# Optimization experiments

Measured on AMD Instinct MI355X. Metric: run time of the kernel, lower is better.

## Reference

```python
import jax, jax.numpy as jnp
import numpy as np
from jax.scipy.special import logsumexp

B, DK, N, M = 16, 512, 1024, 1024
SINKHORN_ITERS = 5
EPS = 1e-8


def setup_inputs() -> dict:
    key = jax.random.key(0)
    k1, k2, k3, k4, k5 = jax.random.split(key, 5)
    return {
        "src_embedding": jax.random.normal(k1, (B, DK, N), dtype=jnp.float32),
        "tgt_embedding": jax.random.normal(k2, (B, DK, M), dtype=jnp.float32),
        "src": jax.random.normal(k3, (B, 3, N), dtype=jnp.float32),
        "tgt": jax.random.normal(k4, (B, 3, M), dtype=jnp.float32),
        # temperature must be positive; uniform in [0.05, 1.0)
        "temperature": jax.random.uniform(k5, (B,), dtype=jnp.float32, minval=0.05, maxval=1.0),
    }


def sinkhorn(scores, n_iters):
    # ZeroPad2d((0,1,0,1)): pad one slack row and one slack column with zeros
    scores = jnp.pad(scores, ((0, 0), (0, 1), (0, 1)))
    for _ in range(n_iters):
        # row normalization (all rows except slack row)
        top = scores[:, :-1, :] - logsumexp(scores[:, :-1, :], axis=2, keepdims=True)
        scores = jnp.concatenate([top, scores[:, -1:, :]], axis=1)
        # column normalization (all cols except slack col)
        left = scores[:, :, :-1] - logsumexp(scores[:, :, :-1], axis=1, keepdims=True)
        scores = jnp.concatenate([left, scores[:, :, -1:]], axis=2)
    return scores[:, :-1, :-1]


def reference(src_embedding, tgt_embedding, src, tgt, temperature):
    b, d_k, n = src_embedding.shape
    # [B, N, M] similarity scores
    dists = jnp.einsum('bdn,bdm->bnm', src_embedding, tgt_embedding) / jnp.sqrt(jnp.float32(d_k))
    affinity = dists / temperature[:, None, None]
    log_perm = sinkhorn(affinity, SINKHORN_ITERS)
    perm = jnp.exp(log_perm)                                             # [B,N,M]
    perm_norm = perm / (jnp.sum(perm, axis=2, keepdims=True) + EPS)      # [B,N,M]
    # soft correspondence: weighted_tgt[b,:,i] = sum_j perm_norm[b,i,j] * tgt[b,:,j]
    weighted_tgt = jnp.einsum('bdm,bnm->bdn', tgt, perm_norm)            # [B,3,N]
    weights = jnp.sum(perm, axis=-1, keepdims=True)                      # [B,N,1]
    weights_norm = weights / (jnp.sum(weights, axis=1, keepdims=True) + EPS)
    weights_norm = jnp.swapaxes(weights_norm, 1, 2)                      # [B,1,N]
    src_centroid = jnp.sum(src * weights_norm, axis=2, keepdims=True)    # [B,3,1]
    tgt_centroid = jnp.sum(weighted_tgt * weights_norm, axis=2, keepdims=True)
    src_centered = src - src_centroid
    corr_centered = (weighted_tgt - tgt_centroid) * weights_norm
    # weighted cross-covariance, batched 3x3
    H = jnp.einsum('bin,bjn->bij', src_centered, corr_centered)          # [B,3,3]
    # batched Procrustes via SVD (torch.svd: H = u diag(s) v^T; jnp: H = u diag(s) vh)
    u, s, vh = jnp.linalg.svd(H)
    v = jnp.swapaxes(vh, 1, 2)
    ut = jnp.swapaxes(u, 1, 2)
    r = jnp.matmul(v, ut)
    r_det = jnp.linalg.det(r)                                            # [B]
    diag = jnp.stack([jnp.ones_like(r_det), jnp.ones_like(r_det), r_det], axis=-1)  # [B,3]
    R = jnp.matmul(v * diag[:, None, :], ut)                             # [B,3,3]
    t = (jnp.matmul(-R, src_centroid) + tgt_centroid).reshape(b, 3)
    return R, t, perm_norm
```

## Files before the change

### kernel.cpp

```cpp
#include <hip/hip_runtime.h>
#include <math.h>

#define BB 16
#define NN 1024
#define MM 1024
#define DKK 512
#define RBLK 16
#define NRB  (NN/RBLK)

typedef short short8 __attribute__((ext_vector_type(8)));
typedef float f32x4 __attribute__((ext_vector_type(4)));

__device__ float g_u[BB*NN];
__device__ float g_v[BB*MM];
__device__ float g_w[BB*NN];
__device__ float g_wt[BB*3*NN];
__device__ float g_pm[BB*NRB*MM];
__device__ float g_ps[BB*NRB*MM];
__device__ __attribute__((aligned(16))) unsigned short gAh[BB*NN*DKK];
__device__ __attribute__((aligned(16))) unsigned short gAl[BB*NN*DKK];
__device__ __attribute__((aligned(16))) unsigned short gBh[BB*MM*DKK];
__device__ __attribute__((aligned(16))) unsigned short gBl[BB*MM*DKK];

__global__ __launch_bounds__(256) void zero_v_kernel() {
    int i = blockIdx.x*256 + threadIdx.x;
    if (i < BB*MM) g_v[i] = 0.0f;
}

__device__ __forceinline__ unsigned int bf16_rne(float x){
    unsigned int u = __float_as_uint(x);
    return (u + 0x7fffu + ((u>>16)&1u)) >> 16;
}

__device__ __forceinline__ void gl_lds(const void* g, void* l){
    __builtin_amdgcn_global_load_lds(
        (const __attribute__((address_space(1))) unsigned int*)g,
        (__attribute__((address_space(3))) unsigned int*)l, 16, 0, 0);
}

__global__ __launch_bounds__(256) void convert_split(const float* __restrict__ A,
                                                     const float* __restrict__ Bm) {
    int z = blockIdx.z;
    int which = z >> 4;
    int b = z & 15;
    const float* X = which ? Bm : A;
    unsigned short* Hh = which ? gBh : gAh;
    unsigned short* Hl = which ? gBl : gAl;
    int d0 = blockIdx.y * 64;
    int i0 = blockIdx.x * 64;
    __shared__ float T[64*65];
    const float* Xb = X + ((size_t)b*DKK + d0)*NN + i0;
    int t = threadIdx.x;
#pragma unroll
    for (int it=0; it<4; ++it){
        int lin = t + 256*it;
        int d = lin >> 4;
        int i4 = lin & 15;
        float4 v = *(const float4*)(Xb + (size_t)d*NN + i4*4);
        T[(i4*4+0)*65 + d] = v.x;
        T[(i4*4+1)*65 + d] = v.y;
        T[(i4*4+2)*65 + d] = v.z;
        T[(i4*4+3)*65 + d] = v.w;
    }
    __syncthreads();
    size_t obase = ((size_t)b*NN + i0)*DKK + d0;
#pragma unroll
    for (int it=0; it<2; ++it){
        int c = t + 256*it;
        int i = c >> 3;
        int p = c & 7;
        unsigned int hw[4], lw[4];
#pragma unroll
        for (int j=0;j<4;j++){
            float x0 = T[i*65 + p*8 + 2*j];
            float x1 = T[i*65 + p*8 + 2*j+1];
            unsigned int h0 = bf16_rne(x0);
            unsigned int h1 = bf16_rne(x1);
            float hf0 = __uint_as_float(h0<<16);
            float hf1 = __uint_as_float(h1<<16);
            unsigned int l0 = bf16_rne(x0 - hf0);
            unsigned int l1 = bf16_rne(x1 - hf1);
            hw[j] = h0 | (h1<<16);
            lw[j] = l0 | (l1<<16);
        }
        int pw = (p & 4) | ((p + (i>>1)) & 3);
        size_t eo = obase + (size_t)i*DKK + pw*8;
        uint4 hv; hv.x=hw[0]; hv.y=hw[1]; hv.z=hw[2]; hv.w=hw[3];
        uint4 lv; lv.x=lw[0]; lv.y=lw[1]; lv.z=lw[2]; lv.w=lw[3];
        *(uint4*)(Hh + eo) = hv;
        *(uint4*)(Hl + eo) = lv;
    }
}

__global__ __launch_bounds__(256) void gemm_mfma(const float* __restrict__ temp,
                                                 float* __restrict__ C) {
    int id   = blockIdx.x;
    int xcd  = id & 7;
    int slot = id >> 3;
    int b    = xcd*2 + (slot >> 6);
    int sub  = slot & 63;
    int i0   = (sub >> 3) << 7;
    int j0   = (sub & 7) << 7;
    __shared__ __attribute__((aligned(16))) char lds[65536];
    int t = threadIdx.x;
    int lane = t & 63, w = t >> 6;
    int wr = w >> 1, wc = w & 1;
    const size_t ebytes = (size_t)b * NN * DKK * 2;

    const char* src[8];
    int dstoff[8];
    {
        int rql = lane >> 2, cl = lane & 3;
#pragma unroll
        for (int o=0;o<4;o++){
            const char* g = (o==0) ? (const char*)gAh : (o==1) ? (const char*)gAl
                           : (o==2) ? (const char*)gBh : (const char*)gBl;
            int t0 = (o<2) ? i0 : j0;
#pragma unroll
            for (int q=0;q<2;q++){
                int rloc = w*32 + q*16 + rql;
                src[o*2+q] = g + ebytes + (size_t)(t0 + rloc)*1024 + cl*16;
                dstoff[o*2+q] = o*8192 + (w*32 + q*16)*64;
            }
        }
    }

    f32x4 acc[16];
#pragma unroll
    for (int q=0;q<16;q++) acc[q] = (f32x4){0.f,0.f,0.f,0.f};

    int fslot = ((lane>>4) + ((lane&15)>>1)) & 3;
    int arow = wr*64 + (lane&15);
    int brow = wc*64 + (lane&15);
    int faoff = arow*64 + fslot*16;
    int fboff = 16384 + brow*64 + fslot*16;

#pragma unroll
    for (int idx=0;idx<8;idx++) gl_lds(src[idx], lds + dstoff[idx]);

    for (int ks=0; ks<16; ++ks){
        __syncthreads();
        int cur = (ks & 1) * 32768;
        if (ks+1 < 16){
            int nxt = ((ks+1) & 1) * 32768;
#pragma unroll
            for (int idx=0;idx<8;idx++){
                src[idx] += 64;
                gl_lds(src[idx], lds + nxt + dstoff[idx]);
            }
        }
        const char* fa = lds + cur + faoff;
        const char* fb = lds + cur + fboff;

        short8 ah[4], bh[4];
#pragma unroll
        for (int mf=0;mf<4;mf++) ah[mf] = *(const short8*)(fa + mf*1024);
#pragma unroll
        for (int nf=0;nf<4;nf++) bh[nf] = *(const short8*)(fb + nf*1024);
#pragma unroll
        for (int nf=0;nf<4;nf++)
#pragma unroll
            for (int mf=0;mf<4;mf++)
                acc[mf*4+nf] = __builtin_amdgcn_mfma_f32_16x16x32_bf16(ah[mf], bh[nf], acc[mf*4+nf], 0,0,0);

        short8 al[4];
#pragma unroll
        for (int mf=0;mf<4;mf++) al[mf] = *(const short8*)(fa + 8192 + mf*1024);
#pragma unroll
        for (int nf=0;nf<4;nf++)
#pragma unroll
            for (int mf=0;mf<4;mf++)
                acc[mf*4+nf] = __builtin_amdgcn_mfma_f32_16x16x32_bf16(al[mf], bh[nf], acc[mf*4+nf], 0,0,0);

        short8 bl[4];
#pragma unroll
        for (int nf=0;nf<4;nf++) bl[nf] = *(const short8*)(fb + 8192 + nf*1024);
#pragma unroll
        for (int nf=0;nf<4;nf++)
#pragma unroll
            for (int mf=0;mf<4;mf++)
                acc[mf*4+nf] = __builtin_amdgcn_mfma_f32_16x16x32_bf16(ah[mf], bl[nf], acc[mf*4+nf], 0,0,0);
    }

    float scale = 1.0f/(22.62741699796952f * temp[b]);
    float* Cb = C + ((size_t)b<<20);
    int r0c = i0 + wr*64 + ((lane>>4)<<2);
    int c0c = j0 + wc*64 + (lane&15);
#pragma unroll
    for (int mf=0;mf<4;mf++){
#pragma unroll
        for (int r2=0;r2<4;r2++){
            float* rowp = Cb + (size_t)(r0c + mf*16 + r2)*MM + c0c;
#pragma unroll
            for (int nf=0;nf<4;nf++)
                rowp[nf*16] = acc[mf*4+nf][r2]*scale;
        }
    }
}

__global__ __launch_bounds__(256) void sink_iter(const float* __restrict__ S) {
    int b   = blockIdx.y;
    int rb  = blockIdx.x;
    int row0 = rb*RBLK;
    int t = threadIdx.x;
    __shared__ float Ls[RBLK*1028];
    __shared__ float v_l[1024];
    __shared__ float u_l[RBLK];

    float4 v4 = *(const float4*)(g_v + (b<<10) + t*4);
    *(float4*)(v_l + t*4) = v4;

    const float* Sb = S + ((size_t)b*NN + row0)*MM;
#pragma unroll
    for (int rr=0; rr<RBLK; ++rr){
        float4 s4 = *(const float4*)(Sb + (size_t)rr*MM + t*4);
        s4.x -= v4.x; s4.y -= v4.y; s4.z -= v4.z; s4.w -= v4.w;
        *(float4*)(&Ls[rr*1028 + t*4]) = s4;
    }
    __syncthreads();

    {
        int r = t >> 4, c = t & 15;
        const float* Lr = &Ls[r*1028 + c];
        float m = -INFINITY;
#pragma unroll
        for (int k=0;k<64;k++) m = fmaxf(m, Lr[16*k]);
#pragma unroll
        for (int off=1; off<16; off<<=1) m = fmaxf(m, __shfl_xor(m, off));
        m = fmaxf(m, 0.0f);
        float s = 0.0f;
#pragma unroll
        for (int k=0;k<64;k++) s += __expf(Lr[16*k] - m);
#pragma unroll
        for (int off=1; off<16; off<<=1) s += __shfl_xor(s, off);
        s += __expf(-m);
        float u = m + __logf(s);
        if (c==0){ u_l[r] = u; g_u[b*NN + row0 + r] = u; }
    }
    __syncthreads();

    float mm[4], ss[4];
#pragma unroll
    for (int q=0;q<4;q++){ mm[q]=-INFINITY; ss[q]=0.f; }
#pragma unroll
    for (int r=0;r<RBLK;++r){
        float ur = u_l[r];
        const float* Lr = &Ls[r*1028];
#pragma unroll
        for (int q=0;q<4;q++)
            mm[q] = fmaxf(mm[q], Lr[t + 256*q] - ur);
    }
#pragma unroll
    for (int r=0;r<RBLK;++r){
        float ur = u_l[r];
        const float* Lr = &Ls[r*1028];
#pragma unroll
        for (int q=0;q<4;q++)
            ss[q] += __expf(Lr[t + 256*q] - ur - mm[q]);
    }
    size_t pbase = ((size_t)(b*NRB + rb) << 10) + t;
#pragma unroll
    for (int q=0;q<4;q++){
        g_pm[pbase + 256*q] = mm[q] + v_l[t + 256*q];
        g_ps[pbase + 256*q] = ss[q];
    }
}

__global__ __launch_bounds__(256) void col_lse_combine() {
    int idx = blockIdx.x*256 + threadIdx.x;
    int b = idx >> 10; int j = idx & (MM-1);
    float m = -INFINITY, s = 0.0f;
    size_t base = ((size_t)(b*NRB) << 10) + j;
    for (int c=0;c<NRB;c++){
        float om = g_pm[base + ((size_t)c<<10)];
        float os = g_ps[base + ((size_t)c<<10)];
        float nm = fmaxf(m, om);
        s = s*__expf(m-nm) + os*__expf(om-nm);
        m = nm;
    }
    float nm = fmaxf(m, 0.0f);
    s = s*__expf(m-nm) + __expf(-nm);
    g_v[idx] = nm + __logf(s);
}

__global__ __launch_bounds__(256) void finalize_rows(float* __restrict__ S,
                                                     const float* __restrict__ tgt) {
    int row  = blockIdx.x*4 + (threadIdx.x>>6);
    int lane = threadIdx.x & 63;
    int b = row >> 10;
    int i = row & (NN-1);
    float ui = g_u[row];
    float4* srow = (float4*)(S + (size_t)row*MM);
    const float4* vb = (const float4*)(g_v + (b<<10));
    const float4* t0 = (const float4*)(tgt + (size_t)b*3*MM);
    const float4* t1 = (const float4*)(tgt + (size_t)b*3*MM + MM);
    const float4* t2 = (const float4*)(tgt + (size_t)b*3*MM + 2*MM);
    float p[16];
    float rs=0.f, a0=0.f, a1=0.f, a2=0.f;
#pragma unroll
    for (int k=0;k<4;k++){
        float4 s4 = srow[lane + 64*k];
        float4 v4 = vb[lane + 64*k];
        p[4*k+0] = __expf(s4.x - ui - v4.x);
        p[4*k+1] = __expf(s4.y - ui - v4.y);
        p[4*k+2] = __expf(s4.z - ui - v4.z);
        p[4*k+3] = __expf(s4.w - ui - v4.w);
        rs += p[4*k+0]+p[4*k+1]+p[4*k+2]+p[4*k+3];
        float4 w0 = t0[lane + 64*k];
        float4 w1 = t1[lane + 64*k];
        float4 w2 = t2[lane + 64*k];
        a0 += p[4*k+0]*w0.x + p[4*k+1]*w0.y + p[4*k+2]*w0.z + p[4*k+3]*w0.w;
        a1 += p[4*k+0]*w1.x + p[4*k+1]*w1.y + p[4*k+2]*w1.z + p[4*k+3]*w1.w;
        a2 += p[4*k+0]*w2.x + p[4*k+1]*w2.y + p[4*k+2]*w2.z + p[4*k+3]*w2.w;
    }
    for (int off=32; off; off>>=1){
        rs += __shfl_xor(rs, off);
        a0 += __shfl_xor(a0, off);
        a1 += __shfl_xor(a1, off);
        a2 += __shfl_xor(a2, off);
    }
    float inv = 1.0f/(rs + 1e-8f);
#pragma unroll
    for (int k=0;k<4;k++){
        srow[lane + 64*k] = make_float4(p[4*k+0]*inv, p[4*k+1]*inv, p[4*k+2]*inv, p[4*k+3]*inv);
    }
    if (lane==0){
        g_w[row] = rs;
        g_wt[(b*3+0)*NN + i] = a0*inv;
        g_wt[(b*3+1)*NN + i] = a1*inv;
        g_wt[(b*3+2)*NN + i] = a2*inv;
    }
}

__global__ __launch_bounds__(256) void procrustes(const float* __restrict__ src,
                                                  float* __restrict__ out) {
    int b = blockIdx.x;
    int t = threadIdx.x;
    __shared__ float red[256];
    auto bsum = [&](float v)->float{
        red[t]=v; __syncthreads();
        for (int o=128;o>0;o>>=1){ if(t<o) red[t]+=red[t+o]; __syncthreads(); }
        float r=red[0]; __syncthreads(); return r;
    };
    const float* wrow = g_w + b*NN;
    float pw=0.f;
    for (int i=t;i<NN;i+=256) pw += wrow[i];
    float W = bsum(pw);
    float winv = 1.0f/(W + 1e-8f);
    const float* sb  = src  + (size_t)b*3*NN;
    const float* wtb = g_wt + (size_t)b*3*NN;
    float sc[3], tc[3];
    for (int c=0;c<3;c++){
        float p1=0.f,p2=0.f;
        for (int i=t;i<NN;i+=256){
            float wn = wrow[i]*winv;
            p1 += sb[c*NN+i]*wn;
            p2 += wtb[c*NN+i]*wn;
        }
        sc[c]=bsum(p1);
        tc[c]=bsum(p2);
    }
    float H[9];
    for (int c=0;c<3;c++)
        for (int d=0;d<3;d++){
            float p=0.f;
            for (int i=t;i<NN;i+=256){
                float wn = wrow[i]*winv;
                p += (sb[c*NN+i]-sc[c]) * ((wtb[d*NN+i]-tc[d])*wn);
            }
            H[c*3+d]=bsum(p);
        }
    if (t==0){
        double Hd[3][3];
        for (int r2=0;r2<3;r2++) for (int c2=0;c2<3;c2++) Hd[r2][c2]=H[r2*3+c2];
        double K[3][3];
        for (int i2=0;i2<3;i2++)
            for (int j2=0;j2<3;j2++){
                double acc=0;
                for (int r2=0;r2<3;r2++) acc += Hd[r2][i2]*Hd[r2][j2];
                K[i2][j2]=acc;
            }
        double V[3][3]={{1,0,0},{0,1,0},{0,0,1}};
        const int PQ[3][2]={{0,1},{0,2},{1,2}};
        for (int sweep=0; sweep<30; ++sweep){
            double off = fabs(K[0][1])+fabs(K[0][2])+fabs(K[1][2]);
            if (off < 1e-26) break;
            for (int pi=0; pi<3; ++pi){
                int p = PQ[pi][0], q = PQ[pi][1];
                double apq = K[p][q];
                if (fabs(apq) < 1e-300) continue;
                double tau = (K[q][q]-K[p][p])/(2.0*apq);
                double tt  = (tau>=0.0?1.0:-1.0)/(fabs(tau)+sqrt(1.0+tau*tau));
                double c   = 1.0/sqrt(1.0+tt*tt);
                double s   = tt*c;
                double Kpp=K[p][p], Kqq=K[q][q];
                K[p][p] = Kpp - tt*apq;
                K[q][q] = Kqq + tt*apq;
                K[p][q] = 0.0; K[q][p] = 0.0;
                int r2 = 3-p-q;
                double Krp=K[r2][p], Krq=K[r2][q];
                K[r2][p] = c*Krp - s*Krq; K[p][r2]=K[r2][p];
                K[r2][q] = s*Krp + c*Krq; K[q][r2]=K[r2][q];
                for (int rr=0; rr<3; ++rr){
                    double vp=V[rr][p], vq=V[rr][q];
                    V[rr][p] = c*vp - s*vq;
                    V[rr][q] = s*vp + c*vq;
                }
            }
        }
        double lam[3]={K[0][0],K[1][1],K[2][2]};
        int o0=0,o1=1,o2=2,tmp;
        if (lam[o0]<lam[o1]){tmp=o0;o0=o1;o1=tmp;}
        if (lam[o0]<lam[o2]){tmp=o0;o0=o2;o2=tmp;}
        if (lam[o1]<lam[o2]){tmp=o1;o1=o2;o2=tmp;}
        int ord[3]={o0,o1,o2};
        double Vs[3][3], U[3][3];
        for (int k=0;k<3;k++)
            for (int r2=0;r2<3;r2++) Vs[r2][k]=V[r2][ord[k]];
        for (int k=0;k<3;k++){
            double ux = Hd[0][0]*Vs[0][k] + Hd[0][1]*Vs[1][k] + Hd[0][2]*Vs[2][k];
            double uy = Hd[1][0]*Vs[0][k] + Hd[1][1]*Vs[1][k] + Hd[1][2]*Vs[2][k];
            double uz = Hd[2][0]*Vs[0][k] + Hd[2][1]*Vs[1][k] + Hd[2][2]*Vs[2][k];
            double n = sqrt(ux*ux+uy*uy+uz*uz);
            if (n > 1e-30){ U[0][k]=ux/n; U[1][k]=uy/n; U[2][k]=uz/n; }
            else {
                double cx = U[1][0]*U[2][1]-U[2][0]*U[1][1];
                double cy = U[2][0]*U[0][1]-U[0][0]*U[2][1];
                double cz = U[0][0]*U[1][1]-U[1][0]*U[0][1];
                U[0][k]=cx; U[1][k]=cy; U[2][k]=cz;
            }
        }
        double rm[3][3];
        for (int i2=0;i2<3;i2++)
            for (int j2=0;j2<3;j2++)
                rm[i2][j2] = Vs[i2][0]*U[j2][0] + Vs[i2][1]*U[j2][1] + Vs[i2][2]*U[j2][2];
        double det = rm[0][0]*(rm[1][1]*rm[2][2]-rm[1][2]*rm[2][1])
                   - rm[0][1]*(rm[1][0]*rm[2][2]-rm[1][2]*rm[2][0])
                   + rm[0][2]*(rm[1][0]*rm[2][1]-rm[1][1]*rm[2][0]);
        double R[3][3];
        for (int i2=0;i2<3;i2++)
            for (int j2=0;j2<3;j2++)
                R[i2][j2] = Vs[i2][0]*U[j2][0] + Vs[i2][1]*U[j2][1] + det*Vs[i2][2]*U[j2][2];
        double tv[3];
        for (int i2=0;i2<3;i2++)
            tv[i2] = -(R[i2][0]*sc[0]+R[i2][1]*sc[1]+R[i2][2]*sc[2]) + tc[i2];
        for (int i2=0;i2<3;i2++)
            for (int j2=0;j2<3;j2++)
                out[b*9 + i2*3 + j2] = (float)R[i2][j2];
        for (int i2=0;i2<3;i2++)
            out[144 + b*3 + i2] = (float)tv[i2];
    }
}

extern "C" void kernel_launch(void* const* d_in, const int* in_sizes, int n_in,
                              void* d_out, int out_size, void* d_ws, size_t ws_size,
                              hipStream_t stream) {
    const float* src_emb = (const float*)d_in[0];
    const float* tgt_emb = (const float*)d_in[1];
    const float* src     = (const float*)d_in[2];
    const float* tgt     = (const float*)d_in[3];
    const float* temp    = (const float*)d_in[4];
    float* out = (float*)d_out;
    float* S = out + 192;

    hipLaunchKernelGGL(zero_v_kernel, dim3(64), dim3(256), 0, stream);
    hipLaunchKernelGGL(convert_split, dim3(16,8,32), dim3(256), 0, stream, src_emb, tgt_emb);
    hipLaunchKernelGGL(gemm_mfma, dim3(1024), dim3(256), 0, stream, temp, S);
    for (int it=0; it<5; ++it){
        hipLaunchKernelGGL(sink_iter, dim3(NRB,BB), dim3(256), 0, stream, S);
        hipLaunchKernelGGL(col_lse_combine, dim3(64), dim3(256), 0, stream);
    }
    hipLaunchKernelGGL(finalize_rows, dim3(4096), dim3(256), 0, stream, S, tgt);
    hipLaunchKernelGGL(procrustes, dim3(16), dim3(256), 0, stream, src, out);
}
```

Baseline: 360.1 us.

## Keep sinkhorn row tiles in registers and parallelize column LSE combine

After: 372.5 us. 3.4% more time.

```diff
diff --git a/kernel.cpp b/kernel.cpp
--- a/kernel.cpp
+++ b/kernel.cpp
@@ -5,7 +5,7 @@
 #define NN 1024
 #define MM 1024
 #define DKK 512
-#define RBLK 16
+#define RBLK 8
 #define NRB  (NN/RBLK)
 
 typedef short short8 __attribute__((ext_vector_type(8)));
@@ -199,88 +199,104 @@
 }
 
 __global__ __launch_bounds__(256) void sink_iter(const float* __restrict__ S) {
-    int b   = blockIdx.y;
-    int rb  = blockIdx.x;
+    int b  = blockIdx.y;
+    int rb = blockIdx.x;
     int row0 = rb*RBLK;
     int t = threadIdx.x;
-    __shared__ float Ls[RBLK*1028];
-    __shared__ float v_l[1024];
-    __shared__ float u_l[RBLK];
+    int w = t >> 6, lane = t & 63;
+    __shared__ float red_m[RBLK][4];
+    __shared__ float red_s[RBLK][4];
 
     float4 v4 = *(const float4*)(g_v + (b<<10) + t*4);
-    *(float4*)(v_l + t*4) = v4;
-
     const float* Sb = S + ((size_t)b*NN + row0)*MM;
-#pragma unroll
-    for (int rr=0; rr<RBLK; ++rr){
-        float4 s4 = *(const float4*)(Sb + (size_t)rr*MM + t*4);
-        s4.x -= v4.x; s4.y -= v4.y; s4.z -= v4.z; s4.w -= v4.w;
-        *(float4*)(&Ls[rr*1028 + t*4]) = s4;
+    float4 x[RBLK];
+#pragma unroll
+    for (int r=0;r<RBLK;++r){
+        float4 s4 = *(const float4*)(Sb + (size_t)r*MM + t*4);
+        x[r].x = s4.x - v4.x; x[r].y = s4.y - v4.y;
+        x[r].z = s4.z - v4.z; x[r].w = s4.w - v4.w;
+    }
+#pragma unroll
+    for (int r=0;r<RBLK;++r){
+        float m = fmaxf(fmaxf(x[r].x,x[r].y), fmaxf(x[r].z,x[r].w));
+#pragma unroll
+        for (int off=32; off; off>>=1) m = fmaxf(m, __shfl_xor(m, off));
+        if (lane==0) red_m[r][w] = m;
     }
     __syncthreads();
-
-    {
-        int r = t >> 4, c = t & 15;
-        const float* Lr = &Ls[r*1028 + c];
-        float m = -INFINITY;
-#pragma unroll
-        for (int k=0;k<64;k++) m = fmaxf(m, Lr[16*k]);
-#pragma unroll
-        for (int off=1; off<16; off<<=1) m = fmaxf(m, __shfl_xor(m, off));
-        m = fmaxf(m, 0.0f);
-        float s = 0.0f;
-#pragma unroll
-        for (int k=0;k<64;k++) s += __expf(Lr[16*k] - m);
-#pragma unroll
-        for (int off=1; off<16; off<<=1) s += __shfl_xor(s, off);
-        s += __expf(-m);
-        float u = m + __logf(s);
-        if (c==0){ u_l[r] = u; g_u[b*NN + row0 + r] = u; }
+    float um[RBLK];
+#pragma unroll
+    for (int r=0;r<RBLK;++r)
+        um[r] = fmaxf(fmaxf(fmaxf(red_m[r][0],red_m[r][1]),
+                            fmaxf(red_m[r][2],red_m[r][3])), 0.0f);
+#pragma unroll
+    for (int r=0;r<RBLK;++r){
+        float s = __expf(x[r].x-um[r]) + __expf(x[r].y-um[r])
+                + __expf(x[r].z-um[r]) + __expf(x[r].w-um[r]);
+#pragma unroll
+        for (int off=32; off; off>>=1) s += __shfl_xor(s, off);
+        if (lane==0) red_s[r][w] = s;
     }
     __syncthreads();
-
-    float mm[4], ss[4];
-#pragma unroll
-    for (int q=0;q<4;q++){ mm[q]=-INFINITY; ss[q]=0.f; }
-#pragma unroll
-    for (int r=0;r<RBLK;++r){
-        float ur = u_l[r];
-        const float* Lr = &Ls[r*1028];
-#pragma unroll
-        for (int q=0;q<4;q++)
-            mm[q] = fmaxf(mm[q], Lr[t + 256*q] - ur);
-    }
-#pragma unroll
-    for (int r=0;r<RBLK;++r){
-        float ur = u_l[r];
-        const float* Lr = &Ls[r*1028];
-#pragma unroll
-        for (int q=0;q<4;q++)
-            ss[q] += __expf(Lr[t + 256*q] - ur - mm[q]);
-    }
-    size_t pbase = ((size_t)(b*NRB + rb) << 10) + t;
-#pragma unroll
-    for (int q=0;q<4;q++){
-        g_pm[pbase + 256*q] = mm[q] + v_l[t + 256*q];
-        g_ps[pbase + 256*q] = ss[q];
-    }
+    float u[RBLK];
+#pragma unroll
+    for (int r=0;r<RBLK;++r){
+        float s = red_s[r][0]+red_s[r][1]+red_s[r][2]+red_s[r][3] + __expf(-um[r]);
+        u[r] = um[r] + __logf(s);
+        if (t == r) g_u[b*NN + row0 + r] = u[r];
+    }
+    float4 cm = make_float4(-INFINITY,-INFINITY,-INFINITY,-INFINITY);
+#pragma unroll
+    for (int r=0;r<RBLK;++r){
+        cm.x = fmaxf(cm.x, x[r].x - u[r]);
+        cm.y = fmaxf(cm.y, x[r].y - u[r]);
+        cm.z = fmaxf(cm.z, x[r].z - u[r]);
+        cm.w = fmaxf(cm.w, x[r].w - u[r]);
+    }
+    float4 cs = make_float4(0.f,0.f,0.f,0.f);
+#pragma unroll
+    for (int r=0;r<RBLK;++r){
+        cs.x += __expf(x[r].x - u[r] - cm.x);
+        cs.y += __expf(x[r].y - u[r] - cm.y);
+        cs.z += __expf(x[r].z - u[r] - cm.z);
+        cs.w += __expf(x[r].w - u[r] - cm.w);
+    }
+    size_t pbase = (((size_t)(b*NRB + rb)) << 10) + t*4;
+    *(float4*)(g_pm + pbase) = make_float4(cm.x+v4.x, cm.y+v4.y, cm.z+v4.z, cm.w+v4.w);
+    *(float4*)(g_ps + pbase) = cs;
 }
 
 __global__ __launch_bounds__(256) void col_lse_combine() {
-    int idx = blockIdx.x*256 + threadIdx.x;
-    int b = idx >> 10; int j = idx & (MM-1);
+    int slice = blockIdx.x;
+    int b     = blockIdx.y;
+    int t = threadIdx.x;
+    int c64 = t & 63, part = t >> 6;
+    int j = slice*64 + c64;
+    __shared__ float sm[4][64], ss[4][64];
     float m = -INFINITY, s = 0.0f;
-    size_t base = ((size_t)(b*NRB) << 10) + j;
-    for (int c=0;c<NRB;c++){
-        float om = g_pm[base + ((size_t)c<<10)];
-        float os = g_ps[base + ((size_t)c<<10)];
+    size_t base = (((size_t)b*NRB) << 10) + j;
+    for (int k=part*32; k<part*32+32; ++k){
+        float om = g_pm[base + ((size_t)k<<10)];
+        float os = g_ps[base + ((size_t)k<<10)];
         float nm = fmaxf(m, om);
         s = s*__expf(m-nm) + os*__expf(om-nm);
         m = nm;
     }
-    float nm = fmaxf(m, 0.0f);
-    s = s*__expf(m-nm) + __expf(-nm);
-    g_v[idx] = nm + __logf(s);
+    sm[part][c64] = m; ss[part][c64] = s;
+    __syncthreads();
+    if (t < 64){
+        float M = sm[0][t], Sv = ss[0][t];
+#pragma unroll
+        for (int p=1;p<4;p++){
+            float om = sm[p][t], os = ss[p][t];
+            float nm = fmaxf(M, om);
+            Sv = Sv*__expf(M-nm) + os*__expf(om-nm);
+            M = nm;
+        }
+        float nm = fmaxf(M, 0.0f);
+        Sv = Sv*__expf(M-nm) + __expf(-nm);
+        g_v[(b<<10) + slice*64 + t] = nm + __logf(Sv);
+    }
 }
 
 __global__ __launch_bounds__(256) void finalize_rows(float* __restrict__ S,
@@ -468,7 +484,7 @@
     hipLaunchKernelGGL(gemm_mfma, dim3(1024), dim3(256), 0, stream, temp, S);
     for (int it=0; it<5; ++it){
         hipLaunchKernelGGL(sink_iter, dim3(NRB,BB), dim3(256), 0, stream, S);
-        hipLaunchKernelGGL(col_lse_combine, dim3(64), dim3(256), 0, stream);
+        hipLaunchKernelGGL(col_lse_combine, dim3(16,16), dim3(256), 0, stream);
     }
     hipLaunchKernelGGL(finalize_rows, dim3(4096), dim3(256), 0, stream, S, tgt);
     hipLaunchKernelGGL(procrustes, dim3(16), dim3(256), 0, stream, src, out);
```
